# Optimization experiments

Measured on AMD Instinct MI355X. Metric: run time of the kernel, lower is better.

## Reference

```python
import math
import jax, jax.numpy as jnp
import numpy as np

B, C, H, W, ATTR = 4, 1024, 16, 8, 21

def setup_inputs() -> dict:
    key = jax.random.key(0)
    ks = jax.random.split(key, 7)
    rn = lambda k, shape, s=1.0: jax.random.normal(k, shape, dtype=jnp.float32) * s
    return {
        "feature": rn(ks[0], (B, C, H, W)),
        "Q": rn(ks[1], (B, C, ATTR)),                 # self.Q parameter
        "W1": rn(ks[2], (C, C), 0.02),                # conv1x1 linear_1 weight [out,in]
        "b1": jnp.zeros((C,), jnp.float32),
        "W2": rn(ks[3], (C, C), 0.02),                # conv1x1 linear_2 weight
        "b2": jnp.zeros((C,), jnp.float32),
        "W3": rn(ks[4], (ATTR * C, ATTR * C), 0.005), # linear_3 weight (bias=False)
        "fc_w": rn(ks[5], (1, C), 0.02),              # fc weight
        "fc_b": jnp.zeros((1,), jnp.float32),
    }

def reference(feature, Q, W1, b1, W2, b2, W3, fc_w, fc_b):
    b, c, h, w = feature.shape
    attr = Q.shape[-1]
    f = feature.reshape(b, c, h * w)                      # [b,c,n]
    # 1x1 convs == per-pixel linear over channels
    lf1 = jnp.einsum('oc,bcn->bon', W1, f) + b1[None, :, None]
    lf2 = jnp.einsum('oc,bcn->bon', W2, f) + b2[None, :, None]
    # linear_3 on flattened self.Q (nn.Linear: x @ W.T)
    lq = (Q.reshape(b, -1) @ W3.T).reshape(b, c, attr)    # [b,c,attr]
    Qp = jnp.transpose(lq, (0, 2, 1))                      # [b,attr,c]
    QK = jnp.einsum('bic,bcn->bin', Qp, lf1) / math.sqrt(c)  # [b,attr,n]
    A = jax.nn.softmax(QK, axis=1)                         # softmax over attr dim (dim=1, as in torch)
    ff = jnp.einsum('bin,bcn->bic', A, lf2)                # [b,attr,c]
    # NOTE: the original loops ssca_forward head_num=3 times, but ssca_forward
    # ignores its Q argument (always reads self.Q), so all 3 iterations produce
    # the identical tensor; one pass is mathematically equivalent.
    pred = (ff @ fc_w.T + fc_b)[..., 0]                    # [b,attr]
    return pred
```

## Files before the change

kernel.cpp:

```cpp
#include <hip/hip_runtime.h>

#define K3   21504
#define C_   1024
#define NPIX 128
#define NATTR 21
#define NB   4
#define ROWS 14

typedef float f32x4 __attribute__((ext_vector_type(4)));

__device__ __forceinline__ float wave_reduce_sum(float v) {
  #pragma unroll
  for (int off = 32; off > 0; off >>= 1)
    v += __shfl_xor(v, off, 64);
  return v;
}


#define LOAD_TILE(W_, Q_, kk)                                          \
  {                                                                    \
    _Pragma("unroll")                                                  \
    for (int r = 0; r < ROWS; ++r)                                     \
      W_[r] = __builtin_nontemporal_load(                              \
                 (const f32x4*)(r0 + (size_t)r * K3 + (kk)));          \
    _Pragma("unroll")                                                  \
    for (int b = 0; b < NB; ++b)                                       \
      Q_[b] = *(const f32x4*)(Q + (size_t)b * K3 + (kk));              \
  }

#define FMA_TILE(W_, Q_)                                               \
  {                                                                    \
    _Pragma("unroll")                                                  \
    for (int r = 0; r < ROWS; ++r)                                     \
      _Pragma("unroll")                                                \
      for (int b = 0; b < NB; ++b) {                                   \
        _Pragma("unroll")                                              \
        for (int e = 0; e < 4; ++e)                                    \
          acc[r][b] += W_[r][e] * Q_[b][e];                            \
      }                                                                \
  }

__global__ __launch_bounds__(64) void k_lq(
    const float* __restrict__ Q, const float* __restrict__ W3,
    float* __restrict__ lq) {
  const int lane = threadIdx.x;
  const int o0 = blockIdx.x * ROWS;
  const float* r0 = W3 + (size_t)o0 * K3;
  float acc[ROWS][NB];
  #pragma unroll
  for (int r = 0; r < ROWS; ++r)
    #pragma unroll
    for (int b = 0; b < NB; ++b) acc[r][b] = 0.f;

  f32x4 wA[ROWS], qA[NB], wB[ROWS], qB[NB];
  int k = lane * 4;
  LOAD_TILE(wA, qA, k);
  #pragma unroll 1
  for (int it = 0; it < 41; ++it) {
    LOAD_TILE(wB, qB, k + 256);
    FMA_TILE(wA, qA);
    LOAD_TILE(wA, qA, k + 512);
    FMA_TILE(wB, qB);
    k += 512;
  }
  LOAD_TILE(wB, qB, k + 256);
  FMA_TILE(wA, qA);
  FMA_TILE(wB, qB);

  #pragma unroll
  for (int r = 0; r < ROWS; ++r)
    #pragma unroll
    for (int b = 0; b < NB; ++b) {
      float s = wave_reduce_sum(acc[r][b]);
      if (lane == 0) lq[(size_t)b * K3 + o0 + r] = s;
    }
}

__global__ __launch_bounds__(256) void k_vu(
    const float* __restrict__ W1, const float* __restrict__ W2,
    const float* __restrict__ lq, const float* __restrict__ fc_w,
    const float* __restrict__ b1, const float* __restrict__ b2,
    float* __restrict__ vu, float* __restrict__ dc) {
  const int blk = blockIdx.x;
  if (blk >= 85 * 16) {
    const int xjob = blk - 85 * 16;
    if (threadIdx.x < 64) {
      const int lane = threadIdx.x;
      float acc = 0.f;
      if (xjob < NB * NATTR) {
        const int b = xjob / NATTR, i = xjob % NATTR;
        for (int c = lane; c < C_; c += 64)
          acc += lq[(size_t)b * K3 + c * NATTR + i] * b1[c];
      } else {
        for (int c = lane; c < C_; c += 64)
          acc += fc_w[c] * b2[c];
      }
      acc = wave_reduce_sum(acc);
      if (lane == 0) dc[xjob] = acc;
    }
    return;
  }
  const int job = blk >> 4;
  const int kc  = blk & 15;
  const int cg  = threadIdx.x >> 6;
  const int kl  = threadIdx.x & 63;
  const int k   = kc * 64 + kl;
  const float* M;
  const float* coef;
  int cstride;
  if (job < NB * NATTR) {
    M = W1;
    coef = lq + (size_t)(job / NATTR) * K3 + (job % NATTR);
    cstride = NATTR;
  } else {
    M = W2;
    coef = fc_w;
    cstride = 1;
  }
  float acc = 0.f;
  const int c0 = cg * 256;
  #pragma unroll 8
  for (int c = c0; c < c0 + 256; ++c)
    acc += coef[c * cstride] * M[(size_t)c * C_ + k];
  __shared__ float red[4][64];
  red[cg][kl] = acc;
  __syncthreads();
  if (threadIdx.x < 64) {
    float s = red[0][kl] + red[1][kl] + red[2][kl] + red[3][kl];
    vu[(size_t)job * C_ + k] = s;
  }
}

__global__ __launch_bounds__(256) void k_attn(
    const float* __restrict__ f, const float* __restrict__ vu,
    const float* __restrict__ dc, float* __restrict__ P) {
  const int b = blockIdx.x >> 7;
  const int n = blockIdx.x & 127;
  const int t = threadIdx.x;
  const int wave = t >> 6, lane = t & 63;
  __shared__ float xs[C_];
  __shared__ float red[22][4];
  #pragma unroll
  for (int j = 0; j < 4; ++j) {
    int c = t + j * 256;
    xs[c] = f[((size_t)b * C_ + c) * NPIX + n];
  }
  __syncthreads();
  for (int ii = 0; ii < 22; ++ii) {
    const float* vec = vu + (size_t)((ii < NATTR) ? (b * NATTR + ii) : NB * NATTR) * C_;
    float p = 0.f;
    #pragma unroll
    for (int j = 0; j < 4; ++j) {
      int c = t + j * 256;
      p += xs[c] * vec[c];
    }
    p = wave_reduce_sum(p);
    if (lane == 0) red[ii][wave] = p;
  }
  __syncthreads();
  if (t == 0) {
    float qk[NATTR];
    float m = -1e30f;
    #pragma unroll
    for (int i = 0; i < NATTR; ++i) {
      qk[i] = (red[i][0] + red[i][1] + red[i][2] + red[i][3]
               + dc[b * NATTR + i]) * 0.03125f;
      m = fmaxf(m, qk[i]);
    }
    float g = red[21][0] + red[21][1] + red[21][2] + red[21][3] + dc[NB * NATTR];
    float s = 0.f;
    #pragma unroll
    for (int i = 0; i < NATTR; ++i) { qk[i] = expf(qk[i] - m); s += qk[i]; }
    const float inv = g / s;
    #pragma unroll
    for (int i = 0; i < NATTR; ++i)
      P[(size_t)(b * NATTR + i) * NPIX + n] = qk[i] * inv;
  }
}

__global__ __launch_bounds__(64) void k_pred(
    const float* __restrict__ P, const float* __restrict__ fc_b,
    float* __restrict__ out) {
  const int job = blockIdx.x;
  const int lane = threadIdx.x;
  float acc = P[(size_t)job * NPIX + lane] + P[(size_t)job * NPIX + 64 + lane];
  acc = wave_reduce_sum(acc);
  if (lane == 0) out[job] = acc + fc_b[0];
}

extern "C" void kernel_launch(void* const* d_in, const int* in_sizes, int n_in,
                              void* d_out, int out_size, void* d_ws, size_t ws_size,
                              hipStream_t stream) {
  const float* feature = (const float*)d_in[0];
  const float* Q   = (const float*)d_in[1];
  const float* W1  = (const float*)d_in[2];
  const float* b1  = (const float*)d_in[3];
  const float* W2  = (const float*)d_in[4];
  const float* b2  = (const float*)d_in[5];
  const float* W3  = (const float*)d_in[6];
  const float* fcw = (const float*)d_in[7];
  const float* fcb = (const float*)d_in[8];
  float* out = (float*)d_out;

  float* ws = (float*)d_ws;
  float* lq = ws;
  float* vu = lq + NB * K3;
  float* dc = vu + 85 * C_;
  float* P  = dc + 85;

  hipLaunchKernelGGL(k_lq,   dim3(K3 / ROWS), dim3(64), 0, stream, Q, W3, lq);
  hipLaunchKernelGGL(k_vu,   dim3(85 * 16 + 85), dim3(256), 0, stream,
                     W1, W2, lq, fcw, b1, b2, vu, dc);
  hipLaunchKernelGGL(k_attn, dim3(NB * NPIX), dim3(256), 0, stream, feature, vu, dc, P);
  hipLaunchKernelGGL(k_pred, dim3(NB * NATTR), dim3(64), 0, stream, P, fcb, out);
}
```

Measured before the change: 373.4 us.

## Share Q tiles across two waves via double-buffered LDS in k_lq

k_lq now runs two waves per block, each handling 14 rows of W3, and stages the Q vector chunks cooperatively into a double-buffered shared-memory tile, so Q is read from global memory once per block instead of once per wave. This cuts redundant Q traffic through L2 and frees vector registers previously used for Q prefetch. In exchange it adds a __syncthreads per 256-element chunk and LDS reads, and halves the grid size, which may lower latency hiding for a kernel dominated by streaming W3.

```diff
diff --git a/kernel.cpp b/kernel.cpp
--- a/kernel.cpp
+++ b/kernel.cpp
@@ -6,6 +6,7 @@
 #define NATTR 21
 #define NB   4
 #define ROWS 14
+#define RPB  28
 
 typedef float f32x4 __attribute__((ext_vector_type(4)));
 
@@ -17,18 +18,7 @@
 }
 
 
-#define LOAD_TILE(W_, Q_, kk)                                          \
-  {                                                                    \
-    _Pragma("unroll")                                                  \
-    for (int r = 0; r < ROWS; ++r)                                     \
-      W_[r] = __builtin_nontemporal_load(                              \
-                 (const f32x4*)(r0 + (size_t)r * K3 + (kk)));          \
-    _Pragma("unroll")                                                  \
-    for (int b = 0; b < NB; ++b)                                       \
-      Q_[b] = *(const f32x4*)(Q + (size_t)b * K3 + (kk));              \
-  }
-
-#define FMA_TILE(W_, Q_)                                               \
+#define FMA_TILE(W_)                                                   \
   {                                                                    \
     _Pragma("unroll")                                                  \
     for (int r = 0; r < ROWS; ++r)                                     \
@@ -36,36 +26,94 @@
       for (int b = 0; b < NB; ++b) {                                   \
         _Pragma("unroll")                                              \
         for (int e = 0; e < 4; ++e)                                    \
-          acc[r][b] += W_[r][e] * Q_[b][e];                            \
+          acc[r][b] += W_[r][e] * q[b][e];                             \
       }                                                                \
   }
 
-__global__ __launch_bounds__(64) void k_lq(
+#define LOAD_W(W_, kk)                                                 \
+  {                                                                    \
+    _Pragma("unroll")                                                  \
+    for (int r = 0; r < ROWS; ++r)                                     \
+      W_[r] = __builtin_nontemporal_load(                              \
+                 (const f32x4*)(r0 + (size_t)r * K3 + (kk)));          \
+  }
+
+#define LOAD_Q(bufi)                                                   \
+  f32x4 q[NB];                                                         \
+  {                                                                    \
+    _Pragma("unroll")                                                  \
+    for (int b = 0; b < NB; ++b)                                       \
+      q[b] = *(const f32x4*)&qs[bufi][b][kl];                          \
+  }
+
+__global__ __launch_bounds__(128) void k_lq(
     const float* __restrict__ Q, const float* __restrict__ W3,
     float* __restrict__ lq) {
-  const int lane = threadIdx.x;
-  const int o0 = blockIdx.x * ROWS;
+  const int t = threadIdx.x;
+  const int wave = t >> 6, lane = t & 63;
+  const int o0 = blockIdx.x * RPB + wave * ROWS;
   const float* r0 = W3 + (size_t)o0 * K3;
+  __shared__ float qs[2][NB][256];
+  const int sb = t >> 5;
+  const int so = (t & 31) * 8;
+  const float* qsrc = Q + (size_t)sb * K3 + so;
+  const int kl = lane * 4;
+
   float acc[ROWS][NB];
   #pragma unroll
   for (int r = 0; r < ROWS; ++r)
     #pragma unroll
     for (int b = 0; b < NB; ++b) acc[r][b] = 0.f;
 
-  f32x4 wA[ROWS], qA[NB], wB[ROWS], qB[NB];
-  int k = lane * 4;
-  LOAD_TILE(wA, qA, k);
+  f32x4 wA[ROWS], wB[ROWS];
+
+  {
+    f32x4 s0 = *(const f32x4*)(qsrc);
+    f32x4 s1 = *(const f32x4*)(qsrc + 4);
+    *(f32x4*)&qs[0][sb][so]     = s0;
+    *(f32x4*)&qs[0][sb][so + 4] = s1;
+  }
+  LOAD_W(wA, kl);
+  __syncthreads();
+
   #pragma unroll 1
   for (int it = 0; it < 41; ++it) {
-    LOAD_TILE(wB, qB, k + 256);
-    FMA_TILE(wA, qA);
-    LOAD_TILE(wA, qA, k + 512);
-    FMA_TILE(wB, qB);
-    k += 512;
-  }
-  LOAD_TILE(wB, qB, k + 256);
-  FMA_TILE(wA, qA);
-  FMA_TILE(wB, qB);
+    const int p0 = 2 * it;
+    {
+      f32x4 s0 = *(const f32x4*)(qsrc + (p0 + 1) * 256);
+      f32x4 s1 = *(const f32x4*)(qsrc + (p0 + 1) * 256 + 4);
+      LOAD_W(wB, (p0 + 1) * 256 + kl);
+      LOAD_Q(0);
+      FMA_TILE(wA);
+      *(f32x4*)&qs[1][sb][so]     = s0;
+      *(f32x4*)&qs[1][sb][so + 4] = s1;
+      __syncthreads();
+    }
+    {
+      f32x4 s0 = *(const f32x4*)(qsrc + (p0 + 2) * 256);
+      f32x4 s1 = *(const f32x4*)(qsrc + (p0 + 2) * 256 + 4);
+      LOAD_W(wA, (p0 + 2) * 256 + kl);
+      LOAD_Q(1);
+      FMA_TILE(wB);
+      *(f32x4*)&qs[0][sb][so]     = s0;
+      *(f32x4*)&qs[0][sb][so + 4] = s1;
+      __syncthreads();
+    }
+  }
+  {
+    f32x4 s0 = *(const f32x4*)(qsrc + 83 * 256);
+    f32x4 s1 = *(const f32x4*)(qsrc + 83 * 256 + 4);
+    LOAD_W(wB, 83 * 256 + kl);
+    LOAD_Q(0);
+    FMA_TILE(wA);
+    *(f32x4*)&qs[1][sb][so]     = s0;
+    *(f32x4*)&qs[1][sb][so + 4] = s1;
+    __syncthreads();
+  }
+  {
+    LOAD_Q(1);
+    FMA_TILE(wB);
+  }
 
   #pragma unroll
   for (int r = 0; r < ROWS; ++r)
@@ -208,7 +256,7 @@
   float* dc = vu + 85 * C_;
   float* P  = dc + 85;
 
-  hipLaunchKernelGGL(k_lq,   dim3(K3 / ROWS), dim3(64), 0, stream, Q, W3, lq);
+  hipLaunchKernelGGL(k_lq,   dim3(K3 / RPB), dim3(128), 0, stream, Q, W3, lq);
   hipLaunchKernelGGL(k_vu,   dim3(85 * 16 + 85), dim3(256), 0, stream,
                      W1, W2, lq, fcw, b1, b2, vu, dc);
   hipLaunchKernelGGL(k_attn, dim3(NB * NPIX), dim3(256), 0, stream, feature, vu, dc, P);
```

Measured after the change: 363.2 us. 2.7% less time.
